# Kernel tuning notes

Hardware: AMD Instinct MI355X
Metric: run time of the kernel (lower is better)

## Reference

```python
import jax, jax.numpy as jnp
import numpy as np

PS = 3
B, C, H, W = 4, 256, 64, 64
IMG = 256
_MEAN = np.array([0.485, 0.456, 0.406], dtype=np.float32).reshape(1, 3, 1, 1)
_STD = np.array([0.229, 0.224, 0.225], dtype=np.float32).reshape(1, 3, 1, 1)


def setup_inputs() -> dict:
    key = jax.random.key(0)
    ks = jax.random.split(key, 16)
    d = {
        "dense_features1": jax.random.normal(ks[0], (B, C, H, W), jnp.float32),
        "dense_features2": jax.random.normal(ks[1], (B, C, H, W), jnp.float32),
        "img_ref_hr": jax.random.uniform(ks[2], (B, 3, IMG, IMG), jnp.float32),
        "w1_1": jax.random.normal(ks[3], (64, 3, 3, 3), jnp.float32) * 0.05,
        "b1_1": jnp.zeros((64,), jnp.float32),
        "w1_2": jax.random.normal(ks[4], (64, 64, 3, 3), jnp.float32) * 0.05,
        "b1_2": jnp.zeros((64,), jnp.float32),
        "w2_1": jax.random.normal(ks[5], (128, 64, 3, 3), jnp.float32) * 0.05,
        "b2_1": jnp.zeros((128,), jnp.float32),
        "w2_2": jax.random.normal(ks[6], (128, 128, 3, 3), jnp.float32) * 0.05,
        "b2_2": jnp.zeros((128,), jnp.float32),
        "w3_1": jax.random.normal(ks[7], (256, 128, 3, 3), jnp.float32) * 0.05,
        "b3_1": jnp.zeros((256,), jnp.float32),
    }
    return d


def _conv(x, w, b):
    y = jax.lax.conv_general_dilated(x, w, (1, 1), "SAME",
                                     dimension_numbers=("NCHW", "OIHW", "NCHW"))
    return y + b[None, :, None, None]


def _pool(x):
    return jax.lax.reduce_window(x, -jnp.inf, jax.lax.max, (1, 1, 2, 2), (1, 1, 2, 2), "VALID")


def _vgg(img, w11, b11, w12, b12, w21, b21, w22, b22, w31, b31):
    x = (img - _MEAN) / _STD  # ImageNet input norm (use_input_norm=True)
    r11 = jax.nn.relu(_conv(x, w11, b11))
    x = _pool(jax.nn.relu(_conv(r11, w12, b12)))
    r21 = jax.nn.relu(_conv(x, w21, b21))
    x = _pool(jax.nn.relu(_conv(r21, w22, b22)))
    r31 = jax.nn.relu(_conv(x, w31, b31))
    return r11, r21, r31


def _l2n(f):  # per-pixel channel L2 normalize (F.normalize dim=0, eps=1e-12)
    return f / jnp.maximum(jnp.linalg.norm(f, axis=0, keepdims=True), 1e-12)


def _patches(f):  # (c,h,w) -> (nh*nw, c*PS*PS), row-major patch order
    c, h, w = f.shape
    nh, nw = h - PS + 1, w - PS + 1
    cols = jnp.stack([f[:, i:i + nh, j:j + nw] for i in range(PS) for j in range(PS)], axis=1)
    return cols.reshape(c * PS * PS, nh * nw).T


def _match(fin, fref):
    fin, fref = _l2n(fin), _l2n(fref)
    nh, nw = fin.shape[1] - PS + 1, fin.shape[2] - PS + 1
    p_in = _patches(fin)
    p_ref = _patches(fref)
    p_ref = p_ref / (jnp.linalg.norm(p_ref, axis=1, keepdims=True) + 1e-5)  # is_norm
    corr = p_in @ p_ref.T  # (N_in, N_ref) patch correlation
    return jnp.argmax(corr, axis=1).reshape(nh, nw)


def _index_to_flow(idx):  # (nh,nw) int -> (nh+2, nw+2, 2) float flow
    nh, nw = idx.shape
    fw = (idx % nw).astype(jnp.float32) - jnp.arange(nw, dtype=jnp.float32)[None, :]
    fh = (idx // nw).astype(jnp.float32) - jnp.arange(nh, dtype=jnp.float32)[:, None]
    flow = jnp.stack([fw, fh], axis=-1)
    return jnp.pad(flow, ((0, 2), (0, 2), (0, 0)))


def _shift9(flow, s):  # 9 down/right shifts with zero fill -> (9,H,W,2)
    Hh, Ww, _ = flow.shape
    outs = [jnp.pad(flow, ((i * s, 0), (j * s, 0), (0, 0)))[:Hh, :Ww]
            for i in range(3) for j in range(3)]
    return jnp.stack(outs, axis=0)


def _per_sample(fin, fref):
    flow3 = _index_to_flow(_match(fin, fref))
    off3 = _shift9(flow3, 1)
    flow2 = jnp.repeat(jnp.repeat(flow3, 2, axis=0), 2, axis=1) * 2.0
    off2 = _shift9(flow2, 2)
    flow1 = jnp.repeat(jnp.repeat(flow3, 4, axis=0), 4, axis=1) * 4.0
    off1 = _shift9(flow1, 4)
    return off1, off2, off3


def reference(dense_features1, dense_features2, img_ref_hr,
              w1_1, b1_1, w1_2, b1_2, w2_1, b2_1, w2_2, b2_2, w3_1, b3_1):
    off1, off2, off3 = jax.vmap(_per_sample)(dense_features1, dense_features2)
    r11, r21, r31 = _vgg(img_ref_hr, w1_1, b1_1, w1_2, b1_2, w2_1, b2_1, w2_2, b2_2, w3_1, b3_1)
    # pre_offset['relu1_1'/'relu2_1'/'relu3_1'], img_ref_feat['relu1_1'/'relu2_1'/'relu3_1']
    return (off1, off2, off3, r11, r21, r31)
```

## Files before the change

kernel.cpp:

```cpp
#include <hip/hip_runtime.h>

typedef __attribute__((ext_vector_type(4))) float f32x4;
typedef __attribute__((ext_vector_type(8))) short s16x8;

#define OFF1_OFF 0
#define OFF2_OFF 4718592
#define OFF3_OFF 5898240
#define R11_OFF  6193152
#define R21_OFF  22970368
#define R31_OFF  31358976

__device__ __forceinline__ ushort f2bf(float x) {
  union { float f; uint u; } c; c.f = x;
  uint r = c.u + 0x7FFFu + ((c.u >> 16) & 1u);
  return (ushort)(r >> 16);
}
__device__ __forceinline__ float bfval(ushort h) {
  union { uint u; float f; } c; c.u = ((uint)h) << 16;
  return c.f;
}

__global__ __launch_bounds__(256)
void k_normalize(const float* __restrict__ f1, const float* __restrict__ f2,
                 ushort* __restrict__ n1b, ushort* __restrict__ n2b) {
  __shared__ uint ldsu[64 * 256];
  float* red = (float*)ldsu;
  float* inv = (float*)ldsu + 256;
  const int t = threadIdx.x, x = t & 63, cg = t >> 6;
  const int h = blockIdx.x, b = blockIdx.y;
  const float* in = blockIdx.z ? f2 : f1;
  ushort* op = blockIdx.z ? n2b : n1b;
  const size_t base = (size_t)b * 256 * 4096 + (size_t)h * 64 + x;
  float vals[64];
  float s = 0.f;
  #pragma unroll
  for (int ci = 0; ci < 64; ++ci) {
    float v = in[base + (size_t)(cg * 64 + ci) * 4096];
    vals[ci] = v;
    s = fmaf(v, v, s);
  }
  red[t] = s;
  __syncthreads();
  if (t < 64) {
    float tot = red[t] + red[64 + t] + red[128 + t] + red[192 + t];
    inv[t] = 1.0f / fmaxf(sqrtf(tot), 1e-12f);
  }
  __syncthreads();
  const float iv = inv[x];
  __syncthreads();
  #pragma unroll
  for (int j = 0; j < 32; ++j) {
    float v0 = vals[2 * j] * iv, v1 = vals[2 * j + 1] * iv;
    ushort h0 = f2bf(v0), h1 = f2bf(v1);
    ushort l0 = f2bf(v0 - bfval(h0)), l1 = f2bf(v1 - bfval(h1));
    int cc = (cg << 1) + (j >> 4);
    int i = j & 15;
    int qh = cc * 32 + i, ql = cc * 32 + 16 + i;
    ldsu[x * 256 + (qh ^ (x & 31))] = (uint)h0 | ((uint)h1 << 16);
    ldsu[x * 256 + (ql ^ (x & 31))] = (uint)l0 | ((uint)l1 << 16);
  }
  __syncthreads();
  uint* og = (uint*)(op + ((size_t)b * 4096 + h * 64) * 512);
  #pragma unroll
  for (int it = 0; it < 64; ++it) {
    int idx = it * 256 + t;
    int p = idx >> 8, q = idx & 255;
    og[idx] = ldsu[p * 256 + (q ^ (p & 31))];
  }
}

__global__ __launch_bounds__(256)
void k_pgemm_mfma(const ushort* __restrict__ Ab, const ushort* __restrict__ Bb,
                  float* __restrict__ P) {
  __shared__ __align__(16) ushort As[128 * 64];
  __shared__ __align__(16) ushort Bs[128 * 64];
  const int t = threadIdx.x;
  const int u0 = blockIdx.y * 128, v0 = blockIdx.x * 128;
  const int lane = t & 63, wv = t >> 6;
  const int wm = wv >> 1, wn = wv & 1;
  const int lr = lane & 15, lk = lane >> 4;
  int rowv[4], slotv[4];
  #pragma unroll
  for (int i = 0; i < 4; ++i) { int e = t + i * 256; rowv[i] = e >> 3; slotv[i] = e & 7; }
  s16x8 ra[4], rb[4];
  #pragma unroll
  for (int i = 0; i < 4; ++i) {
    ra[i] = *(const s16x8*)(Ab + ((size_t)(u0 + rowv[i])) * 512 + slotv[i] * 8);
    rb[i] = *(const s16x8*)(Bb + ((size_t)(v0 + rowv[i])) * 512 + slotv[i] * 8);
  }
  f32x4 acc[4][4];
  #pragma unroll
  for (int mt = 0; mt < 4; ++mt)
    #pragma unroll
    for (int nt = 0; nt < 4; ++nt) {
      f32x4 z = {0.f, 0.f, 0.f, 0.f};
      acc[mt][nt] = z;
    }

  #pragma unroll 1
  for (int cc = 0; cc < 8; ++cc) {
    __syncthreads();
    #pragma unroll
    for (int i = 0; i < 4; ++i) {
      *(s16x8*)(As + ((rowv[i] << 3) + (slotv[i] ^ (rowv[i] & 7))) * 8) = ra[i];
      *(s16x8*)(Bs + ((rowv[i] << 3) + (slotv[i] ^ (rowv[i] & 7))) * 8) = rb[i];
    }
    __syncthreads();
    if (cc < 7) {
      #pragma unroll
      for (int i = 0; i < 4; ++i) {
        ra[i] = *(const s16x8*)(Ab + ((size_t)(u0 + rowv[i])) * 512 + (cc + 1) * 64 + slotv[i] * 8);
        rb[i] = *(const s16x8*)(Bb + ((size_t)(v0 + rowv[i])) * 512 + (cc + 1) * 64 + slotv[i] * 8);
      }
    }
    s16x8 ah[4], al[4], bh[4], bl[4];
    #pragma unroll
    for (int mt = 0; mt < 4; ++mt) {
      int row = wm * 64 + mt * 16 + lr;
      ah[mt] = *(const s16x8*)(As + ((row << 3) + (lk ^ (row & 7))) * 8);
      al[mt] = *(const s16x8*)(As + ((row << 3) + ((4 + lk) ^ (row & 7))) * 8);
    }
    #pragma unroll
    for (int nt = 0; nt < 4; ++nt) {
      int row = wn * 64 + nt * 16 + lr;
      bh[nt] = *(const s16x8*)(Bs + ((row << 3) + (lk ^ (row & 7))) * 8);
      bl[nt] = *(const s16x8*)(Bs + ((row << 3) + ((4 + lk) ^ (row & 7))) * 8);
    }
    #pragma unroll
    for (int mt = 0; mt < 4; ++mt)
      #pragma unroll
      for (int nt = 0; nt < 4; ++nt) {
        acc[mt][nt] = __builtin_amdgcn_mfma_f32_16x16x32_bf16(al[mt], bh[nt], acc[mt][nt], 0, 0, 0);
        acc[mt][nt] = __builtin_amdgcn_mfma_f32_16x16x32_bf16(ah[mt], bl[nt], acc[mt][nt], 0, 0, 0);
        acc[mt][nt] = __builtin_amdgcn_mfma_f32_16x16x32_bf16(ah[mt], bh[nt], acc[mt][nt], 0, 0, 0);
      }
  }
  const int plane = ((blockIdx.y * 2 + wm) << 6) + blockIdx.x * 2 + wn;
  float* Pp = P + (size_t)plane * 4096;
  #pragma unroll
  for (int mt = 0; mt < 4; ++mt)
    #pragma unroll
    for (int nt = 0; nt < 4; ++nt) {
      #pragma unroll
      for (int r = 0; r < 4; ++r)
        Pp[(mt * 16 + lk * 4 + r) * 64 + nt * 16 + lr] = acc[mt][nt][r];
    }
}

__global__ __launch_bounds__(256)
void k_corr(const float* __restrict__ P, float* __restrict__ pv,
            int* __restrict__ pi) {
  __shared__ __align__(16) f32x4 Pl[3 * 1024];
  __shared__ float rv[256];
  __shared__ int   ri[256];
  const int t = threadIdx.x;
  const int py = blockIdx.x / 62, qy = blockIdx.x % 62;
  #pragma unroll
  for (int i = 0; i < 12; ++i) {
    int e = t + i * 256;
    int blk = e >> 10, rem = e & 1023;
    int px = rem >> 4, q4 = rem & 15;
    int pidx = (py + blk) * 64 + (qy + blk);
    f32x4 v = *(const f32x4*)(P + (size_t)pidx * 4096 + rem * 4);
    int slot = ((q4 + (px >> 4)) & 15) ^ (px & 15);
    Pl[blk * 1024 + px * 16 + slot] = v;
  }
  __syncthreads();
  const int px = t & 63, cg = t >> 6;
  #pragma unroll
  for (int j = 0; j < 4; ++j) {
    int c = cg * 4 + j;
    int slot = ((c + (px >> 4)) & 15) ^ (px & 15);
    int o = px * 16 + slot;
    Pl[o] = Pl[o] + Pl[1024 + o] + Pl[2048 + o];
  }
  __syncthreads();
  float bv = -3.4e38f; int bq = 0;
  if (px < 62) {
    const int q0 = cg * 16;
    const int nq = (cg < 3) ? 16 : 14;
    const int nch = (cg < 3) ? 5 : 4;
    float f[3][20];
    #pragma unroll
    for (int dj = 0; dj < 3; ++dj) {
      const int row = px + dj;
      const int rr = row >> 4, rm = row & 15;
      #pragma unroll
      for (int cc2 = 0; cc2 < 5; ++cc2) {
        if (cc2 < nch) {
          int c = cg * 4 + cc2;
          int slot = ((c + rr) & 15) ^ rm;
          f32x4 v = Pl[row * 16 + slot];
          f[dj][cc2 * 4 + 0] = v[0];
          f[dj][cc2 * 4 + 1] = v[1];
          f[dj][cc2 * 4 + 2] = v[2];
          f[dj][cc2 * 4 + 3] = v[3];
        }
      }
    }
    #pragma unroll
    for (int l = 0; l < 16; ++l) {
      if (l < nq) {
        float s = f[0][l] + f[1][l + 1] + f[2][l + 2];
        if (s > bv) { bv = s; bq = q0 + l; }
      }
    }
  }
  rv[t] = bv; ri[t] = bq;
  __syncthreads();
  if (t < 62) {
    float v = rv[t]; int q = ri[t];
    #pragma unroll
    for (int g = 1; g < 4; ++g) {
      float v2 = rv[g * 64 + t];
      if (v2 > v) { v = v2; q = ri[g * 64 + t]; }
    }
    const int n = py * 62 + t;
    pv[(size_t)n * 62 + qy] = v;
    pi[(size_t)n * 62 + qy] = qy * 62 + q;
  }
}

__global__ void k_argmax(const float* __restrict__ pv, const int* __restrict__ pi,
                         int* __restrict__ idxf) {
  int tid = blockIdx.x * 256 + threadIdx.x;
  if (tid >= 4 * 3844) return;
  const float* v = pv + (size_t)tid * 62;
  const int*  ii = pi + (size_t)tid * 62;
  float bv = v[0]; int bi = ii[0];
  for (int q = 1; q < 62; ++q) {
    float x = v[q];
    if (x > bv) { bv = x; bi = ii[q]; }
  }
  idxf[tid] = bi;
}

__global__ void k_flow_all(const int* __restrict__ idxf, float* __restrict__ out) {
  int gid = blockIdx.x * 256 + threadIdx.x;
  int Ho, lg, rel = gid;
  float* o;
  if (gid < 2359296)      { Ho = 256; lg = 2; o = out + OFF1_OFF; }
  else if (gid < 2949120) { Ho = 128; lg = 1; o = out + OFF2_OFF; rel -= 2359296; }
  else if (gid < 3096576) { Ho = 64;  lg = 0; o = out + OFF3_OFF; rel -= 2949120; }
  else return;
  const int x = rel % Ho;
  const int y = (rel / Ho) % Ho;
  const int s = (rel / (Ho * Ho)) % 9;
  const int b = rel / (Ho * Ho * 9);
  const int i = s / 3, j = s % 3;
  const int sc = 1 << lg;
  const int yy = y - i * sc, xx = x - j * sc;
  float fw = 0.f, fh = 0.f;
  if (yy >= 0 && xx >= 0) {
    const int r = yy >> lg, c = xx >> lg;
    if (r < 62 && c < 62) {
      const int id = idxf[b * 3844 + r * 62 + c];
      fw = (float)((id % 62 - c) * sc);
      fh = (float)((id / 62 - r) * sc);
    }
  }
  float2 ov = {fw, fh};
  *(float2*)(o + (size_t)rel * 2) = ov;
}

__global__ void k_wprep_all(const float* __restrict__ w12, const float* __restrict__ w21,
                            const float* __restrict__ w22, const float* __restrict__ w31,
                            ushort* __restrict__ o12, ushort* __restrict__ o21,
                            ushort* __restrict__ o22, ushort* __restrict__ o31) {
  int gid = blockIdx.x * 256 + threadIdx.x;
  const float* w; ushort* o; int CIN, rel;
  if (gid < 36864)        { w = w12; o = o12; CIN = 64;  rel = gid; }
  else if (gid < 110592)  { w = w21; o = o21; CIN = 64;  rel = gid - 36864; }
  else if (gid < 258048)  { w = w22; o = o22; CIN = 128; rel = gid - 110592; }
  else if (gid < 552960)  { w = w31; o = o31; CIN = 128; rel = gid - 258048; }
  else return;
  int ci = rel % CIN;
  int r = rel / CIN;
  int tap = r % 9;
  int oc = r / 9;
  o[((size_t)oc * 9 + tap) * CIN + ci] = f2bf(w[((size_t)oc * CIN + ci) * 9 + tap]);
}

__global__ void k_zb(ushort* __restrict__ a11, ushort* __restrict__ p1,
                     ushort* __restrict__ a21, ushort* __restrict__ p2) {
  int gid = blockIdx.x * 256 + threadIdx.x;
  if (gid >= 99072) return;
  int b = gid / 24768, r = gid % 24768;
  ushort* p; int Hp, Wp, C8, u;
  size_t stride;
  if (r < 8224)       { p = a11; Hp = 258; Wp = 258; C8 = 8;  stride = 4260096; u = r; }
  else if (r < 12352) { p = p1;  Hp = 130; Wp = 130; C8 = 8;  stride = 1081600; u = r - 8224; }
  else if (r < 20608) { p = a21; Hp = 130; Wp = 130; C8 = 16; stride = 2163200; u = r - 12352; }
  else                { p = p2;  Hp = 66;  Wp = 66;  C8 = 16; stride = 557568;  u = r - 20608; }
  int pos = u / C8, j = u % C8;
  int row, col;
  if (pos < Wp)            { row = 0;      col = pos; }
  else if (pos < 2 * Wp)   { row = Hp - 1; col = pos - Wp; }
  else { int q = pos - 2 * Wp; row = 1 + (q >> 1); col = (q & 1) ? (Wp - 1) : 0; }
  s16x8 z = {0, 0, 0, 0, 0, 0, 0, 0};
  *(s16x8*)(p + (size_t)b * stride + (((size_t)row * Wp + col) * C8 + j) * 8) = z;
}

__global__ __launch_bounds__(256)
void k_conv11(const float* __restrict__ img0, const float* __restrict__ w,
              const float* __restrict__ bias, float* __restrict__ outF0,
              ushort* __restrict__ outB0) {
  __shared__ float wl[1728];
  __shared__ float bl[64];
  __shared__ uint ob[8192];
  const int t = threadIdx.x;
  const int b = blockIdx.y;
  const float* img = img0 + (size_t)b * 3 * 65536;
  float* outF = outF0 + (size_t)b * 64 * 65536;
  ushort* outB = outB0 + (size_t)b * 4260096;
  for (int i = t; i < 1728; i += 256) wl[i] = w[i];
  if (t < 64) bl[t] = bias[t];
  __syncthreads();
  const int x = t, y = blockIdx.x;
  const float mean[3] = {0.485f, 0.456f, 0.406f};
  const float stdv[3] = {0.229f, 0.224f, 0.225f};
  float v[27];
  #pragma unroll
  for (int c = 0; c < 3; ++c)
    #pragma unroll
    for (int dy = 0; dy < 3; ++dy)
      #pragma unroll
      for (int dx = 0; dx < 3; ++dx) {
        int iy = y + dy - 1, ix = x + dx - 1;
        float val = 0.f;
        if (iy >= 0 && iy < 256 && ix >= 0 && ix < 256)
          val = (img[((size_t)c * 256 + iy) * 256 + ix] - mean[c]) / stdv[c];
        v[c * 9 + dy * 3 + dx] = val;
      }
  const int xs = x & 31;
  #pragma unroll 4
  for (int op = 0; op < 32; ++op) {
    float a0 = bl[2 * op], a1 = bl[2 * op + 1];
    #pragma unroll
    for (int k = 0; k < 27; ++k) a0 = fmaf(wl[(2 * op) * 27 + k], v[k], a0);
    #pragma unroll
    for (int k = 0; k < 27; ++k) a1 = fmaf(wl[(2 * op + 1) * 27 + k], v[k], a1);
    a0 = fmaxf(a0, 0.f); a1 = fmaxf(a1, 0.f);
    outF[((size_t)(2 * op) * 256 + y) * 256 + x] = a0;
    outF[((size_t)(2 * op + 1) * 256 + y) * 256 + x] = a1;
    ob[x * 32 + (op ^ xs)] = (uint)f2bf(a0) | ((uint)f2bf(a1) << 16);
  }
  __syncthreads();
  uint* og = (uint*)(outB + (((size_t)(y + 1) * 258 + 1) << 6));
  #pragma unroll
  for (int it = 0; it < 8; ++it) {
    int g4 = t + it * 256;
    int xx = g4 >> 3;
    int j0 = (g4 & 7) * 4;
    int xs2 = xx & 31;
    uint4 val;
    val.x = ob[xx * 32 + ((j0 + 0) ^ xs2)];
    val.y = ob[xx * 32 + ((j0 + 1) ^ xs2)];
    val.z = ob[xx * 32 + ((j0 + 2) ^ xs2)];
    val.w = ob[xx * 32 + ((j0 + 3) ^ xs2)];
    *(uint4*)(og + (size_t)g4 * 4) = val;
  }
}

template <int CIN, bool POOL, bool WB16>
__global__ __launch_bounds__(256)
void k_mconv(const ushort* __restrict__ inb, const ushort* __restrict__ wB,
             const float* __restrict__ bias, float* __restrict__ outF,
             ushort* __restrict__ outB, int H, int W, int Cout,
             int inStride, int fStride, int bStride, int PW, int POut) {
  __shared__ __align__(16) char lds_raw[33792];
  ushort* As = (ushort*)lds_raw;
  float*  sm = (float*)lds_raw;
  const int t = threadIdx.x;
  const int bz = blockIdx.z;
  inb += (size_t)bz * inStride;
  outF += (size_t)bz * fStride;
  outB += (size_t)bz * bStride;
  const int xtiles = W >> 6;
  const int xt = blockIdx.x % xtiles;
  const int yp = blockIdx.x / xtiles;
  const int x0 = xt << 6, y0 = yp << 1;
  const int ocb = blockIdx.y << 6;
  const int lane = t & 63, wv = t >> 6;
  const int wm = wv >> 1, wn = wv & 1;
  const int lr = lane & 15, lk = lane >> 4;
  constexpr int NC2 = CIN / 64;

  f32x4 acc[4][2];
  #pragma unroll
  for (int mr = 0; mr < 4; ++mr)
    #pragma unroll
    for (int n = 0; n < 2; ++n) {
      f32x4 z = {0.f, 0.f, 0.f, 0.f};
      acc[mr][n] = z;
    }

  #pragma unroll 1
  for (int cc = 0; cc < NC2; ++cc) {
    __syncthreads();
    #pragma unroll
    for (int i = 0; i < 9; ++i) {
      int e = t + i * 256;
      if (e < 2112) {
        int pos = e >> 3;
        int gs = (e & 7) ^ (pos & 7);
        int hy = pos / 66, hx = pos - hy * 66;
        __builtin_amdgcn_global_load_lds(
            (const __attribute__((address_space(1))) void*)(
                inb + ((size_t)(y0 + hy) * PW + x0 + hx) * CIN + cc * 64 + gs * 8),
            (__attribute__((address_space(3))) void*)(As + (size_t)e * 8), 16, 0, 0);
      }
    }
    __syncthreads();
    #pragma unroll 3
    for (int tap = 0; tap < 9; ++tap) {
      const int dy = tap / 3, dx = tap % 3;
      s16x8 b0[2], b1[2];
      #pragma unroll
      for (int n = 0; n < 2; ++n) {
        const ushort* wp =
            wB + ((size_t)(ocb + wn * 32 + n * 16 + lr) * 9 + tap) * CIN + cc * 64 + lk * 8;
        b0[n] = *(const s16x8*)wp;
        b1[n] = *(const s16x8*)(wp + 32);
      }
      #pragma unroll
      for (int mr = 0; mr < 4; ++mr) {
        const int pos = (wm + dy) * 66 + mr * 16 + lr + dx;
        s16x8 a0 = *(const s16x8*)(As + ((pos << 3) + (lk ^ (pos & 7))) * 8);
        s16x8 a1 = *(const s16x8*)(As + ((pos << 3) + ((4 + lk) ^ (pos & 7))) * 8);
        #pragma unroll
        for (int n = 0; n < 2; ++n) {
          acc[mr][n] = __builtin_amdgcn_mfma_f32_16x16x32_bf16(a0, b0[n], acc[mr][n], 0, 0, 0);
          acc[mr][n] = __builtin_amdgcn_mfma_f32_16x16x32_bf16(a1, b1[n], acc[mr][n], 0, 0, 0);
        }
      }
    }
  }
  __syncthreads();
  #pragma unroll
  for (int mr = 0; mr < 4; ++mr)
    #pragma unroll
    for (int n = 0; n < 2; ++n) {
      const int oc = wn * 32 + n * 16 + lr;
      const float bs = bias[ocb + oc];
      #pragma unroll
      for (int r = 0; r < 4; ++r)
        sm[(wm * 64 + mr * 16 + lk * 4 + r) * 65 + oc] =
            fmaxf(acc[mr][n][r] + bs, 0.f);
    }
  __syncthreads();
  if (POOL) {
    #pragma unroll
    for (int i = 0; i < 4; ++i) {
      int e = t + i * 256;
      int op = e & 31, xo = e >> 5;
      int oc0 = op * 2;
      float m0 = fmaxf(fmaxf(sm[(xo * 2) * 65 + oc0], sm[(xo * 2 + 1) * 65 + oc0]),
                       fmaxf(sm[(64 + xo * 2) * 65 + oc0], sm[(64 + xo * 2 + 1) * 65 + oc0]));
      float m1 = fmaxf(fmaxf(sm[(xo * 2) * 65 + oc0 + 1], sm[(xo * 2 + 1) * 65 + oc0 + 1]),
                       fmaxf(sm[(64 + xo * 2) * 65 + oc0 + 1], sm[(64 + xo * 2 + 1) * 65 + oc0 + 1]));
      size_t pos = (size_t)(yp + 1) * POut + (x0 >> 1) + xo + 1;
      ((uint*)outB)[pos * (Cout >> 1) + ((ocb >> 1) + op)] =
          (uint)f2bf(m0) | ((uint)f2bf(m1) << 16);
    }
  } else {
    #pragma unroll
    for (int i = 0; i < 32; ++i) {
      int e = t + i * 256;
      int oc = e >> 7, sp = e & 127;
      outF[((size_t)(ocb + oc) * H + y0 + (sp >> 6)) * W + x0 + (sp & 63)] =
          sm[sp * 65 + oc];
    }
    if (WB16) {
      #pragma unroll
      for (int i = 0; i < 16; ++i) {
        int e = t + i * 256;
        int op = e & 31, sp = e >> 5;
        int oc0 = op * 2;
        float v0 = sm[sp * 65 + oc0], v1 = sm[sp * 65 + oc0 + 1];
        size_t pos = (size_t)(y0 + (sp >> 6) + 1) * POut + x0 + (sp & 63) + 1;
        ((uint*)outB)[pos * (Cout >> 1) + ((ocb >> 1) + op)] =
            (uint)f2bf(v0) | ((uint)f2bf(v1) << 16);
      }
    }
  }
}

extern "C" void kernel_launch(void* const* d_in, const int* in_sizes, int n_in,
                              void* d_out, int out_size, void* d_ws, size_t ws_size,
                              hipStream_t stream) {
  const float* df1 = (const float*)d_in[0];
  const float* df2 = (const float*)d_in[1];
  const float* img = (const float*)d_in[2];
  const float* w11 = (const float*)d_in[3];
  const float* b11 = (const float*)d_in[4];
  const float* w12 = (const float*)d_in[5];
  const float* b12 = (const float*)d_in[6];
  const float* w21 = (const float*)d_in[7];
  const float* b21 = (const float*)d_in[8];
  const float* w22 = (const float*)d_in[9];
  const float* b22 = (const float*)d_in[10];
  const float* w31 = (const float*)d_in[11];
  const float* b31 = (const float*)d_in[12];
  float* out = (float*)d_out;

  int* idxf = (int*)d_ws;
  ushort* w12b = (ushort*)(idxf + 15376);
  ushort* w21b = w12b + 36864;
  ushort* w22b = w21b + 73728;
  ushort* w31b = w22b + 147456;
  float* P = (float*)((char*)d_ws + (size_t)(4 << 20));
  ushort* a11s = (ushort*)P;
  ushort* p1bs = a11s + 17040384;
  ushort* a21s = p1bs + 4326400;
  ushort* p2bs = a21s + 8652800;

  ushort* n1b = (ushort*)(out + R21_OFF);
  ushort* n2b = n1b + 8388608;
  float* pv = out + OFF1_OFF;
  int*   pi = (int*)(out + OFF1_OFF + 953312);

  k_normalize<<<dim3(64, 4, 2), 256, 0, stream>>>(df1, df2, n1b, n2b);
  k_wprep_all<<<2160, 256, 0, stream>>>(w12, w21, w22, w31, w12b, w21b, w22b, w31b);

  for (int b = 0; b < 4; ++b) {
    k_pgemm_mfma<<<dim3(32, 32, 1), 256, 0, stream>>>(
        n1b + (size_t)b * 2097152, n2b + (size_t)b * 2097152, P);
    k_corr<<<3844, 256, 0, stream>>>(P, pv + (size_t)b * 238328,
                                     pi + (size_t)b * 238328);
  }
  k_argmax<<<61, 256, 0, stream>>>(pv, pi, idxf);

  k_zb<<<387, 256, 0, stream>>>(a11s, p1bs, a21s, p2bs);
  k_conv11<<<dim3(256, 4), 256, 0, stream>>>(img, w11, b11, out + R11_OFF, a11s);
  k_mconv<64, true, false><<<dim3(512, 1, 4), 256, 0, stream>>>(
      a11s, w12b, b12, nullptr, p1bs, 256, 256, 64, 4260096, 0, 1081600, 258, 130);
  k_mconv<64, false, true><<<dim3(128, 2, 4), 256, 0, stream>>>(
      p1bs, w21b, b21, out + R21_OFF, a21s, 128, 128, 128, 1081600, 2097152, 2163200, 130, 130);
  k_mconv<128, true, false><<<dim3(128, 2, 4), 256, 0, stream>>>(
      a21s, w22b, b22, nullptr, p2bs, 128, 128, 128, 2163200, 0, 557568, 130, 66);
  k_mconv<128, false, false><<<dim3(32, 4, 4), 256, 0, stream>>>(
      p2bs, w31b, b31, out + R31_OFF, nullptr, 64, 64, 256, 557568, 1048576, 0, 66, 0);

  k_flow_all<<<12096, 256, 0, stream>>>(idxf, out);
}
```

Baseline: 469.9 us.

## Batch correlation GEMM and corr kernels across samples with diagonal XCD-aware block mapping

Replaces the per-sample loop of GEMM and correlation launches with single launches over all four samples, using blockIdx.z for the GEMM and a remapped 1D grid for the correlation kernel. The correlation blocks are reordered by diagonal (py-qy), and the block index is permuted by orig&7, apparently so that blocks sharing P tiles on a diagonal land on the same XCD and reuse L2. Blocks beyond each diagonal's length exit early. This removes launch serialization and gives more parallelism, but needs a 4x larger P workspace (256MB) that overlaps the conv scratch buffers.

Result: faster. 433.8 us (-7.7%).

```diff
diff --git a/kernel.cpp b/kernel.cpp
--- a/kernel.cpp
+++ b/kernel.cpp
@@ -70,11 +70,15 @@
 }
 
 __global__ __launch_bounds__(256)
-void k_pgemm_mfma(const ushort* __restrict__ Ab, const ushort* __restrict__ Bb,
-                  float* __restrict__ P) {
+void k_pgemm_mfma(const ushort* __restrict__ Ab0, const ushort* __restrict__ Bb0,
+                  float* __restrict__ P0) {
   __shared__ __align__(16) ushort As[128 * 64];
   __shared__ __align__(16) ushort Bs[128 * 64];
   const int t = threadIdx.x;
+  const int bz = blockIdx.z;
+  const ushort* Ab = Ab0 + (size_t)bz * 2097152;
+  const ushort* Bb = Bb0 + (size_t)bz * 2097152;
+  float* P = P0 + (size_t)bz * 16777216;
   const int u0 = blockIdx.y * 128, v0 = blockIdx.x * 128;
   const int lane = t & 63, wv = t >> 6;
   const int wm = wv >> 1, wn = wv & 1;
@@ -148,13 +152,26 @@
 }
 
 __global__ __launch_bounds__(256)
-void k_corr(const float* __restrict__ P, float* __restrict__ pv,
-            int* __restrict__ pi) {
+void k_corr(const float* __restrict__ P0, float* __restrict__ pv0,
+            int* __restrict__ pi0) {
   __shared__ __align__(16) f32x4 Pl[3 * 1024];
   __shared__ float rv[256];
   __shared__ int   ri[256];
   const int t = threadIdx.x;
-  const int py = blockIdx.x / 62, qy = blockIdx.x % 62;
+  const int orig = blockIdx.x;
+  const int logical = (orig & 7) * 3813 + (orig >> 3);
+  const int pos = logical % 62;
+  const int r0 = logical / 62;
+  const int dIdx = r0 % 123;
+  const int bz = r0 / 123;
+  const int d = dIdx - 61;
+  const int len = 62 - (d < 0 ? -d : d);
+  if (pos >= len) return;
+  const int py = pos + (d > 0 ? d : 0);
+  const int qy = py - d;
+  const float* P = P0 + (size_t)bz * 16777216;
+  float* pv = pv0 + (size_t)bz * 238328;
+  int*   pi = pi0 + (size_t)bz * 238328;
   #pragma unroll
   for (int i = 0; i < 12; ++i) {
     int e = t + i * 256;
@@ -509,8 +526,8 @@
   ushort* w21b = w12b + 36864;
   ushort* w22b = w21b + 73728;
   ushort* w31b = w22b + 147456;
-  float* P = (float*)((char*)d_ws + (size_t)(4 << 20));
-  ushort* a11s = (ushort*)P;
+  float* P4 = (float*)((char*)d_ws + (size_t)(4 << 20));
+  ushort* a11s = (ushort*)P4;
   ushort* p1bs = a11s + 17040384;
   ushort* a21s = p1bs + 4326400;
   ushort* p2bs = a21s + 8652800;
@@ -523,12 +540,8 @@
   k_normalize<<<dim3(64, 4, 2), 256, 0, stream>>>(df1, df2, n1b, n2b);
   k_wprep_all<<<2160, 256, 0, stream>>>(w12, w21, w22, w31, w12b, w21b, w22b, w31b);
 
-  for (int b = 0; b < 4; ++b) {
-    k_pgemm_mfma<<<dim3(32, 32, 1), 256, 0, stream>>>(
-        n1b + (size_t)b * 2097152, n2b + (size_t)b * 2097152, P);
-    k_corr<<<3844, 256, 0, stream>>>(P, pv + (size_t)b * 238328,
-                                     pi + (size_t)b * 238328);
-  }
+  k_pgemm_mfma<<<dim3(32, 32, 4), 256, 0, stream>>>(n1b, n2b, P4);
+  k_corr<<<30504, 256, 0, stream>>>(P4, pv, pi);
   k_argmax<<<61, 256, 0, stream>>>(pv, pi, idxf);
 
   k_zb<<<387, 256, 0, stream>>>(a11s, p1bs, a21s, p2bs);
```
